# Optimization experiments

Hardware: AMD Instinct MI355X
Metric: run time of the kernel (lower is better)

The kernel has to match this reference:

```python
import jax, jax.numpy as jnp
import numpy as np

N_NODES = 100000


def gcn_conv(x, W, b, src, dst, n):
    h = x @ W  # transform first (PyG GCNConv order), smaller edge traffic
    loops = jnp.arange(n, dtype=src.dtype)
    s = jnp.concatenate([src, loops])
    d = jnp.concatenate([dst, loops])
    deg = jax.ops.segment_sum(jnp.ones_like(d, dtype=h.dtype), d, num_segments=n)
    dinv = jnp.where(deg > 0, jax.lax.rsqrt(deg), 0.0)
    norm = dinv[s] * dinv[d]  # [E+N]
    msg = h[s] * norm[:, None]  # gather + scale
    out = jax.ops.segment_sum(msg, d, num_segments=n)  # scatter-add
    return out + b


def setup_inputs() -> dict:
    key = jax.random.key(0)
    ks = jax.random.split(key, 8)
    x = jax.random.normal(ks[0], (N_NODES, 256), dtype=jnp.float32)
    edge_index = jax.random.randint(ks[1], (2, 1600000), 0, N_NODES, dtype=jnp.int64)
    pos_edge_index = jax.random.randint(ks[2], (2, 200000), 0, N_NODES, dtype=jnp.int64)
    neg_edge_index = jax.random.randint(ks[3], (2, 200000), 0, N_NODES, dtype=jnp.int64)
    W1 = jax.random.normal(ks[4], (256, 128), dtype=jnp.float32) * (1.0 / np.sqrt(256))
    b1 = jnp.zeros((128,), dtype=jnp.float32)
    W2 = jax.random.normal(ks[5], (128, 8), dtype=jnp.float32) * (1.0 / np.sqrt(128))
    b2 = jnp.zeros((8,), dtype=jnp.float32)
    return {"x": x, "edge_index": edge_index, "pos_edge_index": pos_edge_index,
            "neg_edge_index": neg_edge_index, "W1": W1, "b1": b1, "W2": W2, "b2": b2}


def reference(x, edge_index, pos_edge_index, neg_edge_index, W1, b1, W2, b2):
    n = x.shape[0]
    src, dst = edge_index[0], edge_index[1]
    h = jax.nn.relu(gcn_conv(x, W1, b1, src, dst, n))
    z = gcn_conv(h, W2, b2, src, dst, n)  # [N, 8]
    ei = jnp.concatenate([pos_edge_index, neg_edge_index], axis=-1)
    return jnp.sum(z[ei[0]] * z[ei[1]], axis=-1)  # [E_pos + E_neg]
```

## Files before the change

### kernel.cpp

```cpp
#include <hip/hip_runtime.h>

constexpr int N   = 100000;
constexpr int E   = 1600000;
constexpr int EP  = 200000;
constexpr int ES  = 400000;
constexpr int CAP = 64;
constexpr int XG2 = 128;
constexpr int DR2 = (N + XG2 - 1) / XG2;
constexpr int NH  = N / 2;
constexpr int SEGCAP = 14336;
constexpr int EPB = 8192;
constexpr int PBS = 1024;
constexpr int NPB = (E + EPB - 1) / EPB;
constexpr int BSTR = 264;

typedef _Float16 f16x8 __attribute__((ext_vector_type(8)));
typedef _Float16 f16x4 __attribute__((ext_vector_type(4)));
typedef _Float16 f16x2 __attribute__((ext_vector_type(2)));
typedef float    f32x4 __attribute__((ext_vector_type(4)));

__global__ __launch_bounds__(1024) void partition_edges(const int* __restrict__ ei,
                                                        int* __restrict__ gcnt,
                                                        unsigned* __restrict__ eb) {
    __shared__ int lh[XG2];
    __shared__ int rk[XG2];
    const int tid = threadIdx.x;
    const int e0  = blockIdx.x * EPB;
    if (tid < XG2) lh[tid] = 0;
    __syncthreads();
#pragma unroll
    for (int i = 0; i < EPB; i += PBS) {
        const int e = e0 + i + tid;
        if (e < E) {
            const int d = ei[E + e];
            atomicAdd(&lh[d / DR2], 1);
        }
    }
    __syncthreads();
    if (tid < XG2) rk[tid] = atomicAdd(&gcnt[tid], lh[tid]);
    __syncthreads();
#pragma unroll
    for (int i = 0; i < EPB; i += PBS) {
        const int e = e0 + i + tid;
        if (e < E) {
            const int s   = ei[e];
            const int d   = ei[E + e];
            const int g   = d / DR2;
            const int rel = d - g * DR2;
            const int p   = atomicAdd(&rk[g], 1);
            if (p < SEGCAP)
                eb[(size_t)g * SEGCAP + p] = ((unsigned)rel << 17) | (unsigned)s;
        }
    }
}

__global__ __launch_bounds__(1024) void fill_csr(const unsigned* __restrict__ eb,
                                                 const int* __restrict__ gcnt,
                                                 int* __restrict__ cnt,
                                                 int* __restrict__ rp,
                                                 int* __restrict__ colc) {
    __shared__ int hcnt[1024];
    __shared__ int wsum[16];
    __shared__ unsigned stage[SEGCAP];
    const int g   = blockIdx.x;
    const int tid = threadIdx.x;
    const int cg  = min(gcnt[g], SEGCAP);
    const unsigned* seg = eb + (size_t)g * SEGCAP;

    hcnt[tid] = 0;
    __syncthreads();
    for (int i = tid; i < cg; i += 1024)
        atomicAdd(&hcnt[seg[i] >> 17], 1);
    __syncthreads();

    const int c    = hcnt[tid];
    const int lane = tid & 63;
    const int wid  = tid >> 6;
    int incl = c;
#pragma unroll
    for (int off = 1; off < 64; off <<= 1) {
        const int v = __shfl_up(incl, off);
        if (lane >= off) incl += v;
    }
    if (lane == 63) wsum[wid] = incl;
    __syncthreads();
    if (tid < 16) {
        int v = wsum[tid];
#pragma unroll
        for (int off = 1; off < 16; off <<= 1) {
            const int u = __shfl_up(v, off);
            if (tid >= off) v += u;
        }
        wsum[tid] = v;
    }
    __syncthreads();
    const int excl = incl - c + (wid ? wsum[wid - 1] : 0);

    const int base = g * DR2;
    if (tid < DR2 && base + tid < N) {
        cnt[base + tid] = c;
        rp [base + tid] = g * SEGCAP + excl;
    }
    __syncthreads();
    hcnt[tid] = excl;
    __syncthreads();

    for (int i = tid; i < cg; i += 1024) {
        const unsigned pk = seg[i];
        const int p = atomicAdd(&hcnt[pk >> 17], 1);
        stage[p] = pk & 0x1FFFFu;
    }
    __syncthreads();
    for (int i = tid; i < cg; i += 1024)
        colc[(size_t)g * SEGCAP + i] = (int)stage[i];
}

__global__ __launch_bounds__(256) void w1_transpose(const float* __restrict__ W1,
                                                    _Float16* __restrict__ W1T) {
    const int n = blockIdx.x;
    const int k = threadIdx.x;
    W1T[n * 256 + k] = (_Float16)W1[(size_t)k * 128 + n];
}

__global__ __launch_bounds__(256) void gemm1_mfma(const float* __restrict__ X,
                                                  const _Float16* __restrict__ W1T,
                                                  _Float16* __restrict__ H) {
    __shared__ _Float16 Bs[128][BSTR];

    const int tid  = threadIdx.x;
    const int wave = tid >> 6;
    const int lane = tid & 63;
    const int m16  = lane & 15;
    const int quad = lane >> 4;
    const int rowBase = blockIdx.x * 256 + wave * 64;

#pragma unroll
    for (int i = 0; i < 16; ++i) {
        const int c  = tid + 256 * i;
        const int n  = c >> 5;
        const int kb = (c & 31) * 16;
        *(f16x8*)((char*)&Bs[n][0] + kb) = *(const f16x8*)((const char*)W1T + (size_t)c * 16);
    }
    __syncthreads();

    f32x4 acc[4][8] = {};
    f32x4 avA[8];

    auto loadA = [&](int k0) {
#pragma unroll
        for (int m = 0; m < 4; ++m) {
            int gr = rowBase + m * 16 + m16;
            gr = gr < N ? gr : N - 1;
            const f32x4* p = (const f32x4*)&X[(size_t)gr * 256 + k0 + quad * 8];
            avA[2 * m]     = __builtin_nontemporal_load(p);
            avA[2 * m + 1] = __builtin_nontemporal_load(p + 1);
        }
    };

    loadA(0);
    for (int k0 = 0; k0 < 256; k0 += 32) {
        f16x8 af[4];
#pragma unroll
        for (int m = 0; m < 4; ++m) {
            f16x8 h;
            h[0] = (_Float16)avA[2*m][0];   h[1] = (_Float16)avA[2*m][1];
            h[2] = (_Float16)avA[2*m][2];   h[3] = (_Float16)avA[2*m][3];
            h[4] = (_Float16)avA[2*m+1][0]; h[5] = (_Float16)avA[2*m+1][1];
            h[6] = (_Float16)avA[2*m+1][2]; h[7] = (_Float16)avA[2*m+1][3];
            af[m] = h;
        }
        if (k0 + 32 < 256) loadA(k0 + 32);
#pragma unroll
        for (int nt = 0; nt < 8; ++nt) {
            const f16x8 bf = *(const f16x8*)&Bs[nt * 16 + m16][k0 + quad * 8];
#pragma unroll
            for (int m = 0; m < 4; ++m)
                acc[m][nt] = __builtin_amdgcn_mfma_f32_16x16x32_f16(af[m], bf, acc[m][nt], 0, 0, 0);
        }
    }

#pragma unroll
    for (int m = 0; m < 4; ++m)
#pragma unroll
        for (int nt = 0; nt < 8; ++nt)
#pragma unroll
            for (int r = 0; r < 4; ++r) {
                const int gm = rowBase + m * 16 + quad * 4 + r;
                if (gm < N) H[(size_t)gm * 128 + nt * 16 + m16] = (_Float16)acc[m][nt][r];
            }
}

__global__ __launch_bounds__(256) void agg1_gemm2(const _Float16* __restrict__ H,
                                                  const int* __restrict__ cnt,
                                                  const int* __restrict__ rp,
                                                  const int* __restrict__ colc,
                                                  const float* __restrict__ b1,
                                                  const float* __restrict__ W2,
                                                  float* __restrict__ Z,
                                                  int nbase, int ncount) {
    const int nr   = (blockIdx.x * blockDim.x + threadIdx.x) >> 6;
    const int lane = threadIdx.x & 63;
    if (nr >= ncount) return;
    const int n = nbase + nr;
    const int c = min(cnt[n], CAP);
    const int rpn = rp[n];

    int sv = n;
    if (lane < c) sv = colc[rpn + lane];
    const float dvw = rsqrtf((float)cnt[sv] + 1.0f);
    const float dv  = (lane <= c) ? dvw : 0.0f;

    const _Float16* hbase = H + lane * 2;
    const int ned4 = (c + 1 + 3) & ~3;

    f16x2 va[4]; float wa[4];
#pragma unroll
    for (int t = 0; t < 4; ++t) {
        const int   e = min(t, 63);
        const int   s = __shfl(sv, e);
        wa[t]         = __shfl(dv, e);
        va[t] = *(const f16x2*)&hbase[(size_t)s * 128];
    }
    float ax = 0.f, ay = 0.f;
    for (int j = 4; j < ned4; j += 4) {
        f16x2 vb[4]; float wb[4];
#pragma unroll
        for (int t = 0; t < 4; ++t) {
            const int   e = min(j + t, 63);
            const int   s = __shfl(sv, e);
            wb[t]         = __shfl(dv, e);
            vb[t] = *(const f16x2*)&hbase[(size_t)s * 128];
        }
#pragma unroll
        for (int t = 0; t < 4; ++t) {
            ax = fmaf(wa[t], (float)va[t][0], ax);
            ay = fmaf(wa[t], (float)va[t][1], ay);
            va[t] = vb[t]; wa[t] = wb[t];
        }
    }
#pragma unroll
    for (int t = 0; t < 4; ++t) {
        ax = fmaf(wa[t], (float)va[t][0], ax);
        ay = fmaf(wa[t], (float)va[t][1], ay);
    }

    const float dn = __shfl(dv, c);
    const float2 b = *(const float2*)&b1[lane * 2];
    const float hr0 = fmaxf(ax * dn + b.x, 0.f);
    const float hr1 = fmaxf(ay * dn + b.y, 0.f);

    const float4 wa0 = *(const float4*)&W2[(size_t)(lane * 2) * 8];
    const float4 wa1 = *(const float4*)&W2[(size_t)(lane * 2) * 8 + 4];
    const float4 wb0 = *(const float4*)&W2[(size_t)(lane * 2 + 1) * 8];
    const float4 wb1 = *(const float4*)&W2[(size_t)(lane * 2 + 1) * 8 + 4];
    float p[8];
    p[0] = hr0 * wa0.x + hr1 * wb0.x;
    p[1] = hr0 * wa0.y + hr1 * wb0.y;
    p[2] = hr0 * wa0.z + hr1 * wb0.z;
    p[3] = hr0 * wa0.w + hr1 * wb0.w;
    p[4] = hr0 * wa1.x + hr1 * wb1.x;
    p[5] = hr0 * wa1.y + hr1 * wb1.y;
    p[6] = hr0 * wa1.z + hr1 * wb1.z;
    p[7] = hr0 * wa1.w + hr1 * wb1.w;
#pragma unroll
    for (int off = 32; off > 0; off >>= 1)
#pragma unroll
        for (int j = 0; j < 8; ++j) p[j] += __shfl_xor(p[j], off);
    if (lane == 0) {
        *(float4*)&Z[(size_t)n * 8]     = make_float4(p[0], p[1], p[2], p[3]);
        *(float4*)&Z[(size_t)n * 8 + 4] = make_float4(p[4], p[5], p[6], p[7]);
    }
}

__global__ __launch_bounds__(64) void agg2(const float* __restrict__ Z,
                                           const int* __restrict__ cnt,
                                           const int* __restrict__ rp,
                                           const int* __restrict__ colc,
                                           const float* __restrict__ b2,
                                           float* __restrict__ ZA) {
    const int n = blockIdx.x * blockDim.x + threadIdx.x;
    if (n >= N) return;
    const int c = min(cnt[n], CAP);
    const int rpn = rp[n];
    float acc[8] = {};

    float4 va0[4], va1[4]; float wv[4];
#pragma unroll
    for (int t = 0; t < 4; ++t) {
        const int s = (t < c) ? colc[rpn + t] : n;
        wv[t]  = (t < c) ? rsqrtf((float)cnt[s] + 1.0f) : 0.0f;
        va0[t] = *(const float4*)&Z[(size_t)s * 8];
        va1[t] = *(const float4*)&Z[(size_t)s * 8 + 4];
    }
    for (int j = 4; j + 4 <= c + 4; j += 4) {
        float4 vb0[4], vb1[4]; float wb[4];
#pragma unroll
        for (int t = 0; t < 4; ++t) {
            const int jt = j + t;
            const int s  = (jt < c) ? colc[rpn + jt] : n;
            wb[t]  = (jt < c) ? rsqrtf((float)cnt[s] + 1.0f) : 0.0f;
            vb0[t] = *(const float4*)&Z[(size_t)s * 8];
            vb1[t] = *(const float4*)&Z[(size_t)s * 8 + 4];
        }
#pragma unroll
        for (int t = 0; t < 4; ++t) {
            const float w = wv[t];
            acc[0] = fmaf(w, va0[t].x, acc[0]); acc[1] = fmaf(w, va0[t].y, acc[1]);
            acc[2] = fmaf(w, va0[t].z, acc[2]); acc[3] = fmaf(w, va0[t].w, acc[3]);
            acc[4] = fmaf(w, va1[t].x, acc[4]); acc[5] = fmaf(w, va1[t].y, acc[5]);
            acc[6] = fmaf(w, va1[t].z, acc[6]); acc[7] = fmaf(w, va1[t].w, acc[7]);
            va0[t] = vb0[t]; va1[t] = vb1[t]; wv[t] = wb[t];
        }
    }
#pragma unroll
    for (int t = 0; t < 4; ++t) {
        const float w = wv[t];
        acc[0] = fmaf(w, va0[t].x, acc[0]); acc[1] = fmaf(w, va0[t].y, acc[1]);
        acc[2] = fmaf(w, va0[t].z, acc[2]); acc[3] = fmaf(w, va0[t].w, acc[3]);
        acc[4] = fmaf(w, va1[t].x, acc[4]); acc[5] = fmaf(w, va1[t].y, acc[5]);
        acc[6] = fmaf(w, va1[t].z, acc[6]); acc[7] = fmaf(w, va1[t].w, acc[7]);
    }

    const float dn = rsqrtf((float)c + 1.0f);
    const float4 zn0 = *(const float4*)&Z[(size_t)n * 8];
    const float4 zn1 = *(const float4*)&Z[(size_t)n * 8 + 4];
    float o[8];
    o[0] = (acc[0] + dn * zn0.x) * dn + b2[0];
    o[1] = (acc[1] + dn * zn0.y) * dn + b2[1];
    o[2] = (acc[2] + dn * zn0.z) * dn + b2[2];
    o[3] = (acc[3] + dn * zn0.w) * dn + b2[3];
    o[4] = (acc[4] + dn * zn1.x) * dn + b2[4];
    o[5] = (acc[5] + dn * zn1.y) * dn + b2[5];
    o[6] = (acc[6] + dn * zn1.z) * dn + b2[6];
    o[7] = (acc[7] + dn * zn1.w) * dn + b2[7];
    *(float4*)&ZA[(size_t)n * 8]     = make_float4(o[0], o[1], o[2], o[3]);
    *(float4*)&ZA[(size_t)n * 8 + 4] = make_float4(o[4], o[5], o[6], o[7]);
}

__global__ __launch_bounds__(256) void score(const float* __restrict__ ZA,
                                             const int* __restrict__ pe,
                                             const int* __restrict__ ne,
                                             float* __restrict__ out) {
    const int e = blockIdx.x * blockDim.x + threadIdx.x;
    if (e >= ES) return;
    int a, b;
    if (e < EP) { a = pe[e];      b = pe[EP + e]; }
    else        { a = ne[e - EP]; b = ne[e];      }
    const float4 xa0 = *(const float4*)&ZA[(size_t)a * 8];
    const float4 xa1 = *(const float4*)&ZA[(size_t)a * 8 + 4];
    const float4 xb0 = *(const float4*)&ZA[(size_t)b * 8];
    const float4 xb1 = *(const float4*)&ZA[(size_t)b * 8 + 4];
    out[e] = xa0.x * xb0.x + xa0.y * xb0.y + xa0.z * xb0.z + xa0.w * xb0.w +
             xa1.x * xb1.x + xa1.y * xb1.y + xa1.z * xb1.z + xa1.w * xb1.w;
}


extern "C" void kernel_launch(void* const* d_in, const int* in_sizes, int n_in,
                              void* d_out, int out_size, void* d_ws, size_t ws_size,
                              hipStream_t stream) {
    const float* x  = (const float*)d_in[0];
    const int*   ei = (const int*)d_in[1];
    const int*   pe = (const int*)d_in[2];
    const int*   ne = (const int*)d_in[3];
    const float* W1 = (const float*)d_in[4];
    const float* b1 = (const float*)d_in[5];
    const float* W2 = (const float*)d_in[6];
    const float* b2 = (const float*)d_in[7];
    float* out = (float*)d_out;

    char* ws = (char*)d_ws;
    size_t off = 0;
    auto carve = [&](size_t bytes) {
        char* p = ws + off;
        off += (bytes + 255) & ~(size_t)255;
        return p;
    };
    int*       gcnt = (int*)      carve((size_t)XG2 * sizeof(int));
    int*       cnt  = (int*)      carve((size_t)N * sizeof(int));
    int*       rp   = (int*)      carve((size_t)N * sizeof(int));
    unsigned*  eb   = (unsigned*) carve((size_t)XG2 * SEGCAP * sizeof(unsigned));
    int*       colc = (int*)      carve((size_t)XG2 * SEGCAP * sizeof(int));
    _Float16*  H    = (_Float16*) carve((size_t)N * 128 * sizeof(_Float16));
    float*     Z    = (float*)    carve((size_t)N * 8 * sizeof(float));
    float*     ZA   = (float*)    carve((size_t)N * 8 * sizeof(float));
    _Float16*  W1T  = (_Float16*) carve((size_t)128 * 256 * sizeof(_Float16));

    hipMemsetAsync(gcnt, 0, (size_t)XG2 * sizeof(int), stream);
    partition_edges<<<NPB, PBS, 0, stream>>>(ei, gcnt, eb);
    w1_transpose   <<<128, 256, 0, stream>>>(W1, W1T);
    fill_csr       <<<XG2, 1024, 0, stream>>>(eb, gcnt, cnt, rp, colc);
    gemm1_mfma     <<<(N + 255) / 256, 256, 0, stream>>>(x, W1T, H);
    agg1_gemm2     <<<(NH * 64 + 255) / 256, 256, 0, stream>>>(H, cnt, rp, colc, b1, W2, Z, 0, NH);
    agg1_gemm2     <<<((N - NH) * 64 + 255) / 256, 256, 0, stream>>>(H, cnt, rp, colc, b1, W2, Z, NH, N - NH);
    agg2           <<<(N + 63) / 64, 64, 0, stream>>>(Z, cnt, rp, colc, b2, ZA);
    score          <<<(ES + 255) / 256, 256, 0, stream>>>(ZA, pe, ne, out);
}
```

Before: 359.0 us.

## Split agg2 across 8 threads per node and merge agg1 launches

The second aggregation kernel now assigns eight threads to each node, one per output feature, instead of one thread per node handling all eight features. This raises parallelism and makes the feature loads coalesced per node, at the cost of each thread redundantly loading the neighbour indices and degree values. The two half-range agg1_gemm2 launches are also merged into a single launch covering all nodes, removing one kernel launch.

Result: no change. 357.4 us (-0.4%).

```diff
diff --git a/kernel.cpp b/kernel.cpp
--- a/kernel.cpp
+++ b/kernel.cpp
@@ -7,7 +7,6 @@
 constexpr int CAP = 64;
 constexpr int XG2 = 128;
 constexpr int DR2 = (N + XG2 - 1) / XG2;
-constexpr int NH  = N / 2;
 constexpr int SEGCAP = 14336;
 constexpr int EPB = 8192;
 constexpr int PBS = 1024;
@@ -196,12 +195,10 @@
                                                   const int* __restrict__ colc,
                                                   const float* __restrict__ b1,
                                                   const float* __restrict__ W2,
-                                                  float* __restrict__ Z,
-                                                  int nbase, int ncount) {
-    const int nr   = (blockIdx.x * blockDim.x + threadIdx.x) >> 6;
+                                                  float* __restrict__ Z) {
+    const int n    = (blockIdx.x * blockDim.x + threadIdx.x) >> 6;
     const int lane = threadIdx.x & 63;
-    if (nr >= ncount) return;
-    const int n = nbase + nr;
+    if (n >= N) return;
     const int c = min(cnt[n], CAP);
     const int rpn = rp[n];
 
@@ -272,69 +269,48 @@
     }
 }
 
-__global__ __launch_bounds__(64) void agg2(const float* __restrict__ Z,
-                                           const int* __restrict__ cnt,
-                                           const int* __restrict__ rp,
-                                           const int* __restrict__ colc,
-                                           const float* __restrict__ b2,
-                                           float* __restrict__ ZA) {
-    const int n = blockIdx.x * blockDim.x + threadIdx.x;
+__global__ __launch_bounds__(256) void agg2(const float* __restrict__ Z,
+                                            const int* __restrict__ cnt,
+                                            const int* __restrict__ rp,
+                                            const int* __restrict__ colc,
+                                            const float* __restrict__ b2,
+                                            float* __restrict__ ZA) {
+    const int t = blockIdx.x * blockDim.x + threadIdx.x;
+    const int n = t >> 3;
+    const int f = t & 7;
     if (n >= N) return;
-    const int c = min(cnt[n], CAP);
+    const int c   = min(cnt[n], CAP);
     const int rpn = rp[n];
-    float acc[8] = {};
-
-    float4 va0[4], va1[4]; float wv[4];
-#pragma unroll
-    for (int t = 0; t < 4; ++t) {
-        const int s = (t < c) ? colc[rpn + t] : n;
-        wv[t]  = (t < c) ? rsqrtf((float)cnt[s] + 1.0f) : 0.0f;
-        va0[t] = *(const float4*)&Z[(size_t)s * 8];
-        va1[t] = *(const float4*)&Z[(size_t)s * 8 + 4];
+
+    float acc = 0.f;
+    float zv[4], wv[4];
+#pragma unroll
+    for (int tt = 0; tt < 4; ++tt) {
+        const int s = (tt < c) ? colc[rpn + tt] : n;
+        wv[tt] = (tt < c) ? rsqrtf((float)cnt[s] + 1.0f) : 0.0f;
+        zv[tt] = Z[(size_t)s * 8 + f];
     }
     for (int j = 4; j + 4 <= c + 4; j += 4) {
-        float4 vb0[4], vb1[4]; float wb[4];
-#pragma unroll
-        for (int t = 0; t < 4; ++t) {
-            const int jt = j + t;
+        float zb[4], wb[4];
+#pragma unroll
+        for (int tt = 0; tt < 4; ++tt) {
+            const int jt = j + tt;
             const int s  = (jt < c) ? colc[rpn + jt] : n;
-            wb[t]  = (jt < c) ? rsqrtf((float)cnt[s] + 1.0f) : 0.0f;
-            vb0[t] = *(const float4*)&Z[(size_t)s * 8];
-            vb1[t] = *(const float4*)&Z[(size_t)s * 8 + 4];
-        }
-#pragma unroll
-        for (int t = 0; t < 4; ++t) {
-            const float w = wv[t];
-            acc[0] = fmaf(w, va0[t].x, acc[0]); acc[1] = fmaf(w, va0[t].y, acc[1]);
-            acc[2] = fmaf(w, va0[t].z, acc[2]); acc[3] = fmaf(w, va0[t].w, acc[3]);
-            acc[4] = fmaf(w, va1[t].x, acc[4]); acc[5] = fmaf(w, va1[t].y, acc[5]);
-            acc[6] = fmaf(w, va1[t].z, acc[6]); acc[7] = fmaf(w, va1[t].w, acc[7]);
-            va0[t] = vb0[t]; va1[t] = vb1[t]; wv[t] = wb[t];
-        }
-    }
-#pragma unroll
-    for (int t = 0; t < 4; ++t) {
-        const float w = wv[t];
-        acc[0] = fmaf(w, va0[t].x, acc[0]); acc[1] = fmaf(w, va0[t].y, acc[1]);
-        acc[2] = fmaf(w, va0[t].z, acc[2]); acc[3] = fmaf(w, va0[t].w, acc[3]);
-        acc[4] = fmaf(w, va1[t].x, acc[4]); acc[5] = fmaf(w, va1[t].y, acc[5]);
-        acc[6] = fmaf(w, va1[t].z, acc[6]); acc[7] = fmaf(w, va1[t].w, acc[7]);
-    }
+            wb[tt] = (jt < c) ? rsqrtf((float)cnt[s] + 1.0f) : 0.0f;
+            zb[tt] = Z[(size_t)s * 8 + f];
+        }
+#pragma unroll
+        for (int tt = 0; tt < 4; ++tt) {
+            acc = fmaf(wv[tt], zv[tt], acc);
+            zv[tt] = zb[tt]; wv[tt] = wb[tt];
+        }
+    }
+#pragma unroll
+    for (int tt = 0; tt < 4; ++tt) acc = fmaf(wv[tt], zv[tt], acc);
 
     const float dn = rsqrtf((float)c + 1.0f);
-    const float4 zn0 = *(const float4*)&Z[(size_t)n * 8];
-    const float4 zn1 = *(const float4*)&Z[(size_t)n * 8 + 4];
-    float o[8];
-    o[0] = (acc[0] + dn * zn0.x) * dn + b2[0];
-    o[1] = (acc[1] + dn * zn0.y) * dn + b2[1];
-    o[2] = (acc[2] + dn * zn0.z) * dn + b2[2];
-    o[3] = (acc[3] + dn * zn0.w) * dn + b2[3];
-    o[4] = (acc[4] + dn * zn1.x) * dn + b2[4];
-    o[5] = (acc[5] + dn * zn1.y) * dn + b2[5];
-    o[6] = (acc[6] + dn * zn1.z) * dn + b2[6];
-    o[7] = (acc[7] + dn * zn1.w) * dn + b2[7];
-    *(float4*)&ZA[(size_t)n * 8]     = make_float4(o[0], o[1], o[2], o[3]);
-    *(float4*)&ZA[(size_t)n * 8 + 4] = make_float4(o[4], o[5], o[6], o[7]);
+    const float zn = Z[(size_t)n * 8 + f];
+    ZA[(size_t)n * 8 + f] = (acc + dn * zn) * dn + b2[f];
 }
 
 __global__ __launch_bounds__(256) void score(const float* __restrict__ ZA,
@@ -390,8 +366,7 @@
     w1_transpose   <<<128, 256, 0, stream>>>(W1, W1T);
     fill_csr       <<<XG2, 1024, 0, stream>>>(eb, gcnt, cnt, rp, colc);
     gemm1_mfma     <<<(N + 255) / 256, 256, 0, stream>>>(x, W1T, H);
-    agg1_gemm2     <<<(NH * 64 + 255) / 256, 256, 0, stream>>>(H, cnt, rp, colc, b1, W2, Z, 0, NH);
-    agg1_gemm2     <<<((N - NH) * 64 + 255) / 256, 256, 0, stream>>>(H, cnt, rp, colc, b1, W2, Z, NH, N - NH);
-    agg2           <<<(N + 63) / 64, 64, 0, stream>>>(Z, cnt, rp, colc, b2, ZA);
+    agg1_gemm2     <<<((size_t)N * 64 + 255) / 256, 256, 0, stream>>>(H, cnt, rp, colc, b1, W2, Z);
+    agg2           <<<((size_t)N * 8 + 255) / 256, 256, 0, stream>>>(Z, cnt, rp, colc, b2, ZA);
     score          <<<(ES + 255) / 256, 256, 0, stream>>>(ZA, pe, ne, out);
 }
```
